# Kernel optimization log

Hardware: AMD Instinct MI355X
Metric: run time of the kernel (lower is better)

## Reference

```python
import jax, jax.numpy as jnp
import numpy as np

PATCH = 8
C1 = 1e-4
C2 = 1e-3
EPS = 1e-3
ALPHA = 0.4
WEIGHTS = (1.0, 0.01, 1.0)


def charbonnier(x):
    return (x * x + EPS * EPS) ** ALPHA


def resize_bilinear_ac(img, H2, W2):
    # bilinear resize with align_corners=True (matches F.interpolate)
    B, C, H, W = img.shape
    fy = jnp.arange(H2, dtype=img.dtype) * ((H - 1) / max(H2 - 1, 1))
    fx = jnp.arange(W2, dtype=img.dtype) * ((W - 1) / max(W2 - 1, 1))
    y0 = jnp.clip(jnp.floor(fy).astype(jnp.int32), 0, H - 2)
    x0 = jnp.clip(jnp.floor(fx).astype(jnp.int32), 0, W - 2)
    wy = (fy - y0)[None, None, :, None]
    wx = (fx - x0)[None, None, None, :]
    rows = img[:, :, y0, :] * (1 - wy) + img[:, :, y0 + 1, :] * wy  # [B,C,H2,W]
    out = rows[:, :, :, x0] * (1 - wx) + rows[:, :, :, x0 + 1] * wx  # [B,C,H2,W2]
    return out


def bilinear_warp(img, flow):
    # backward warp: sample img at (x + u, y + v), bilinear, border clamp
    B, C, H, W = img.shape
    gx = jnp.arange(W, dtype=img.dtype)[None, None, :] + flow[:, 0]  # [B,H,W]
    gy = jnp.arange(H, dtype=img.dtype)[None, :, None] + flow[:, 1]  # [B,H,W]
    x0f = jnp.floor(gx)
    y0f = jnp.floor(gy)
    wx = (gx - x0f)[:, None]  # [B,1,H,W]
    wy = (gy - y0f)[:, None]
    x0 = jnp.clip(x0f.astype(jnp.int32), 0, W - 1)
    x1 = jnp.clip(x0 + 1, 0, W - 1)
    y0 = jnp.clip(y0f.astype(jnp.int32), 0, H - 1)
    y1 = jnp.clip(y0 + 1, 0, H - 1)
    imgf = img.reshape(B, C, H * W)

    def gather(yi, xi):
        idx = (yi * W + xi).reshape(B, 1, H * W)
        g = jnp.take_along_axis(imgf, jnp.broadcast_to(idx, (B, C, H * W)), axis=2)
        return g.reshape(B, C, H, W)

    v00 = gather(y0, x0)
    v01 = gather(y0, x1)
    v10 = gather(y1, x0)
    v11 = gather(y1, x1)
    top = v00 * (1 - wx) + v01 * wx
    bot = v10 * (1 - wx) + v11 * wx
    return top * (1 - wy) + bot * wy


def torch_gradient(x, axis):
    # torch.gradient: central diff interior, one-sided at edges, spacing 1
    n = x.shape[axis]
    sl = lambda a, b: jax.lax.slice_in_dim(x, a, b, axis=axis)
    first = sl(1, 2) - sl(0, 1)
    interior = (sl(2, n) - sl(0, n - 2)) * 0.5
    last = sl(n - 1, n) - sl(n - 2, n - 1)
    return jnp.concatenate([first, interior, last], axis=axis)


def ssim_score(I1, I2):
    # faithful to SSIMLoss: stats pooled over ALL non-overlapping patches per
    # (batch, channel), i.e. over the region cropped to multiples of patch.
    B, C, H, W = I1.shape
    p = min(PATCH, H)
    PH, PW = H // p, W // p
    x = I1[:, :, :PH * p, :PW * p].reshape(B, C, -1)
    y = I2[:, :, :PH * p, :PW * p].reshape(B, C, -1)
    N = x.shape[-1]
    mu1 = x.mean(-1)
    mu2 = y.mean(-1)
    d1 = x - mu1[..., None]
    d2 = y - mu2[..., None]
    var1 = (d1 * d1).sum(-1) / (N - 1)  # torch .var() is unbiased
    var2 = (d2 * d2).sum(-1) / (N - 1)
    s12 = (d1 * d2).mean(-1)
    num = (2 * mu1 * mu2 + C1) * (2 * s12 + C2)
    den = (mu1 ** 2 + mu2 ** 2 + C1) * (var1 + var2 + C2)
    return num / den  # [B, C]


def setup_inputs() -> dict:
    key = jax.random.key(0)
    k1, k2 = jax.random.split(key)
    images = jax.random.uniform(k1, (16, 33, 256, 256), dtype=jnp.float32)
    flows = jax.random.normal(k2, (16, 20, 128, 128), dtype=jnp.float32)
    return {"images": images, "flows": flows}


def reference(images, flows):
    B, Cf, FH, FW = flows.shape
    n_flows = Cf // 2  # 10 frame pairs
    imgs = resize_bilinear_ac(images, FH, FW)  # [B,33,FH,FW]
    src = imgs[:, 3:].reshape(B * n_flows, 3, FH, FW)
    fl = flows.reshape(B * n_flows, 2, FH, FW)
    warped = bilinear_warp(src, fl).reshape(B, n_flows * 3, FH, FW)
    ref = imgs[:, : n_flows * 3]

    similarity_loss = ssim_score(ref, warped).mean()

    flow_x = flows[:, 0::2]
    flow_y = flows[:, 1::2]
    smooth = (charbonnier(torch_gradient(flow_x, 1))
              + charbonnier(torch_gradient(flow_x, 2))
              + charbonnier(torch_gradient(flow_y, 1))
              + charbonnier(torch_gradient(flow_y, 2))).mean()

    pixel_loss = charbonnier(ref - warped).mean()

    return WEIGHTS[0] * pixel_loss + WEIGHTS[1] * smooth + WEIGHTS[2] * similarity_loss
```

## Files before the change

### kernel.cpp

```cpp
#include <hip/hip_runtime.h>

#define IH 256
#define IW 256
#define FH 128
#define FW 128
#define NB 16
#define ICH 33
#define NF 10
#define NC 30
#define PL (FH * FW)
#define RES_OFF 4096
#define RES_CNT (NB * ICH * PL)
#define WS_NEED ((size_t)(RES_OFF + RES_CNT) * 4)

__device__ __forceinline__ float charb(float g) {
    float t = fmaf(g, g, 1e-6f);
    return __builtin_amdgcn_exp2f(0.4f * __builtin_amdgcn_logf(t));
}

__device__ __forceinline__ float resized_at(const float* __restrict__ plane, int Y, int X) {
    const float s = (float)(255.0 / 127.0);
    float fy = (float)Y * s;
    float fx = (float)X * s;
    int y0 = (int)fy; y0 = y0 > IH - 2 ? IH - 2 : y0;
    int x0 = (int)fx; x0 = x0 > IW - 2 ? IW - 2 : x0;
    float wy = fy - (float)y0;
    float wx = fx - (float)x0;
    const float* p0 = plane + y0 * IW + x0;
    float v00 = p0[0], v01 = p0[1];
    float v10 = p0[IW], v11 = p0[IW + 1];
    float r0 = v00 * (1.f - wy) + v10 * wy;
    float r1 = v01 * (1.f - wy) + v11 * wy;
    return r0 * (1.f - wx) + r1 * wx;
}

__global__ void __launch_bounds__(256) resize_kernel(const float* __restrict__ images,
                                                     float* __restrict__ resized)
{
    int idx = blockIdx.x * 256 + threadIdx.x;
    int bc = idx >> 14;
    int pix = idx & (PL - 1);
    int h = pix >> 7;
    int w = pix & (FW - 1);
    const float* plane = images + (size_t)bc * (IH * IW);
    resized[idx] = resized_at(plane, h, w);
}

#define SPLIT 4
#define PIX_PER_BLOCK (PL / SPLIT)
__global__ void __launch_bounds__(256) loss_main(const float* __restrict__ resized,
                                                 const float* __restrict__ flows,
                                                 float* __restrict__ acc_bc,
                                                 float* __restrict__ acc_g)
{
    int bc = blockIdx.x / SPLIT;
    int part = blockIdx.x % SPLIT;
    int b = bc / NC;
    int c = bc % NC;
    int f = c / 3;
    const float* ref_plane = resized + (size_t)(b * ICH + c) * PL;
    const float* src_plane = resized + (size_t)(b * ICH + 3 + c) * PL;
    const float* fx_plane  = flows + (size_t)(b * 2 * NF + 2 * f) * PL;
    const float* fy_plane  = fx_plane + PL;

    float s_ref = 0.f, s_w = 0.f, s_r2 = 0.f, s_w2 = 0.f, s_rw = 0.f, s_pix = 0.f;
    int base = part * PIX_PER_BLOCK;
    for (int i = threadIdx.x; i < PIX_PER_BLOCK; i += 256) {
        int pix = base + i;
        int h = pix >> 7;
        int w = pix & (FW - 1);
        float ref = ref_plane[pix];
        float fxv = fx_plane[pix];
        float fyv = fy_plane[pix];
        float gx = (float)w + fxv;
        float gy = (float)h + fyv;
        float x0f = floorf(gx), y0f = floorf(gy);
        float wx = gx - x0f, wy = gy - y0f;
        int x0 = (int)x0f; x0 = min(max(x0, 0), FW - 1);
        int y0 = (int)y0f; y0 = min(max(y0, 0), FH - 1);
        int x1 = min(x0 + 1, FW - 1);
        int y1 = min(y0 + 1, FH - 1);
        const float* r0p = src_plane + y0 * FW;
        const float* r1p = src_plane + y1 * FW;
        float v00 = r0p[x0], v01 = r0p[x1];
        float v10 = r1p[x0], v11 = r1p[x1];
        float top = v00 * (1.f - wx) + v01 * wx;
        float bot = v10 * (1.f - wx) + v11 * wx;
        float wv = top * (1.f - wy) + bot * wy;

        s_ref += ref; s_w += wv;
        s_r2 += ref * ref; s_w2 += wv * wv; s_rw += ref * wv;
        s_pix += charb(ref - wv);
    }
    for (int off = 32; off > 0; off >>= 1) {
        s_ref += __shfl_down(s_ref, off, 64);
        s_w   += __shfl_down(s_w, off, 64);
        s_r2  += __shfl_down(s_r2, off, 64);
        s_w2  += __shfl_down(s_w2, off, 64);
        s_rw  += __shfl_down(s_rw, off, 64);
        s_pix += __shfl_down(s_pix, off, 64);
    }
    __shared__ float sh[4][6];
    int wave = threadIdx.x >> 6;
    if ((threadIdx.x & 63) == 0) {
        sh[wave][0] = s_ref; sh[wave][1] = s_w; sh[wave][2] = s_r2;
        sh[wave][3] = s_w2;  sh[wave][4] = s_rw; sh[wave][5] = s_pix;
    }
    __syncthreads();
    if (threadIdx.x == 0) {
        float t0 = 0, t1 = 0, t2 = 0, t3 = 0, t4 = 0, t5 = 0;
        for (int v = 0; v < 4; v++) {
            t0 += sh[v][0]; t1 += sh[v][1]; t2 += sh[v][2];
            t3 += sh[v][3]; t4 += sh[v][4]; t5 += sh[v][5];
        }
        float* a = acc_bc + bc * 8;
        atomicAdd(a + 0, t0);
        atomicAdd(a + 1, t1);
        atomicAdd(a + 2, t2);
        atomicAdd(a + 3, t3);
        atomicAdd(a + 4, t4);
        atomicAdd(acc_g + 0, t5);
    }
}

__global__ void __launch_bounds__(256) smooth_kernel(const float* __restrict__ flows,
                                                     float* __restrict__ acc_g)
{
    const int total = NB * NF * PL;
    float s = 0.f;
    for (int i = blockIdx.x * blockDim.x + threadIdx.x; i < total;
         i += gridDim.x * blockDim.x) {
        int w = i & (FW - 1);
        int h = (i >> 7) & (FH - 1);
        int f = (i >> 14) % NF;
        int b = i / (NF * PL);
        int pix = h * FW + w;
        const float* xp = flows + (size_t)(b * 2 * NF + 2 * f) * PL;
        const float* yp = xp + PL;

        float g1x, g1y;
        if (f == 0)           { g1x = xp[2 * PL + pix] - xp[pix];
                                g1y = yp[2 * PL + pix] - yp[pix]; }
        else if (f == NF - 1) { g1x = xp[pix] - xp[pix - 2 * PL];
                                g1y = yp[pix] - yp[pix - 2 * PL]; }
        else                  { g1x = 0.5f * (xp[2 * PL + pix] - xp[pix - 2 * PL]);
                                g1y = 0.5f * (yp[2 * PL + pix] - yp[pix - 2 * PL]); }

        float g2x, g2y;
        if (h == 0)           { g2x = xp[pix + FW] - xp[pix];
                                g2y = yp[pix + FW] - yp[pix]; }
        else if (h == FH - 1) { g2x = xp[pix] - xp[pix - FW];
                                g2y = yp[pix] - yp[pix - FW]; }
        else                  { g2x = 0.5f * (xp[pix + FW] - xp[pix - FW]);
                                g2y = 0.5f * (yp[pix + FW] - yp[pix - FW]); }

        s += charb(g1x) + charb(g2x) + charb(g1y) + charb(g2y);
    }
    for (int off = 32; off > 0; off >>= 1) s += __shfl_down(s, off, 64);
    __shared__ float sh[4];
    int wave = threadIdx.x >> 6;
    if ((threadIdx.x & 63) == 0) sh[wave] = s;
    __syncthreads();
    if (threadIdx.x == 0)
        atomicAdd(acc_g + 2, sh[0] + sh[1] + sh[2] + sh[3]);
}

__global__ void __launch_bounds__(512) finalize(const float* __restrict__ acc_bc,
                                                const float* __restrict__ acc_g,
                                                float* __restrict__ out)
{
    __shared__ float sh[512];
    int tid = threadIdx.x;
    float ssim = 0.f;
    if (tid < NB * NC) {
        const float* a = acc_bc + tid * 8;
        const float N = (float)PL;
        float mu1 = a[0] / N, mu2 = a[1] / N;
        float var1 = (a[2] - a[0] * mu1) / (N - 1.f);
        float var2 = (a[3] - a[1] * mu2) / (N - 1.f);
        float s12 = a[4] / N - mu1 * mu2;
        float num = (2.f * mu1 * mu2 + 1e-4f) * (2.f * s12 + 1e-3f);
        float den = (mu1 * mu1 + mu2 * mu2 + 1e-4f) * (var1 + var2 + 1e-3f);
        ssim = num / den;
    }
    sh[tid] = ssim;
    __syncthreads();
    for (int off = 256; off > 0; off >>= 1) {
        if (tid < off) sh[tid] += sh[tid + off];
        __syncthreads();
    }
    if (tid == 0) {
        float pix    = acc_g[0] / (float)(NB * NC * PL);
        float smooth = acc_g[2] / (float)(NB * NF * PL);
        float sim    = sh[0] / (float)(NB * NC);
        out[0] = pix + 0.01f * smooth + sim;
    }
}

__global__ void __launch_bounds__(256) loss_main_fb(const float* __restrict__ images,
                                                    const float* __restrict__ flows,
                                                    float* __restrict__ acc_bc,
                                                    float* __restrict__ acc_g)
{
    int bc = blockIdx.x / 8;
    int part = blockIdx.x % 8;
    int b = bc / NC;
    int c = bc % NC;
    int f = c / 3;
    const float* ref_plane = images + (size_t)(b * ICH + c) * (IH * IW);
    const float* src_plane = images + (size_t)(b * ICH + 3 + c) * (IH * IW);
    const float* fx_plane  = flows + (size_t)(b * 2 * NF + 2 * f) * PL;
    const float* fy_plane  = fx_plane + PL;

    float s_ref = 0.f, s_w = 0.f, s_r2 = 0.f, s_w2 = 0.f, s_rw = 0.f, s_pix = 0.f;
    int base = part * (PL / 8);
    for (int i = threadIdx.x; i < PL / 8; i += 256) {
        int pix = base + i;
        int h = pix >> 7;
        int w = pix & (FW - 1);
        float ref = resized_at(ref_plane, h, w);
        float fxv = fx_plane[pix];
        float fyv = fy_plane[pix];
        float gx = (float)w + fxv;
        float gy = (float)h + fyv;
        float x0f = floorf(gx), y0f = floorf(gy);
        float wx = gx - x0f, wy = gy - y0f;
        int x0 = (int)x0f; x0 = min(max(x0, 0), FW - 1);
        int y0 = (int)y0f; y0 = min(max(y0, 0), FH - 1);
        int x1 = min(x0 + 1, FW - 1);
        int y1 = min(y0 + 1, FH - 1);
        float v00 = resized_at(src_plane, y0, x0);
        float v01 = resized_at(src_plane, y0, x1);
        float v10 = resized_at(src_plane, y1, x0);
        float v11 = resized_at(src_plane, y1, x1);
        float top = v00 * (1.f - wx) + v01 * wx;
        float bot = v10 * (1.f - wx) + v11 * wx;
        float wv = top * (1.f - wy) + bot * wy;
        s_ref += ref; s_w += wv;
        s_r2 += ref * ref; s_w2 += wv * wv; s_rw += ref * wv;
        s_pix += charb(ref - wv);
    }
    for (int off = 32; off > 0; off >>= 1) {
        s_ref += __shfl_down(s_ref, off, 64);
        s_w   += __shfl_down(s_w, off, 64);
        s_r2  += __shfl_down(s_r2, off, 64);
        s_w2  += __shfl_down(s_w2, off, 64);
        s_rw  += __shfl_down(s_rw, off, 64);
        s_pix += __shfl_down(s_pix, off, 64);
    }
    if ((threadIdx.x & 63) == 0) {
        float* a = acc_bc + bc * 8;
        atomicAdd(a + 0, s_ref);
        atomicAdd(a + 1, s_w);
        atomicAdd(a + 2, s_r2);
        atomicAdd(a + 3, s_w2);
        atomicAdd(a + 4, s_rw);
        atomicAdd(acc_g + 0, s_pix);
    }
}

extern "C" void kernel_launch(void* const* d_in, const int* in_sizes, int n_in,
                              void* d_out, int out_size, void* d_ws, size_t ws_size,
                              hipStream_t stream) {
    const float* images = (const float*)d_in[0];
    const float* flows  = (const float*)d_in[1];
    float* acc_bc  = (float*)d_ws;
    float* acc_g   = acc_bc + NB * NC * 8;
    float* resized = (float*)d_ws + RES_OFF;
    (void)hipMemsetAsync(d_ws, 0, (NB * NC * 8 + 4) * sizeof(float), stream);
    if (ws_size >= WS_NEED) {
        resize_kernel<<<RES_CNT / 256, 256, 0, stream>>>(images, resized);
        loss_main<<<NB * NC * SPLIT, 256, 0, stream>>>(resized, flows, acc_bc, acc_g);
    } else {
        loss_main_fb<<<NB * NC * 8, 256, 0, stream>>>(images, flows, acc_bc, acc_g);
    }
    smooth_kernel<<<1280, 256, 0, stream>>>(flows, acc_g);
    finalize<<<1, 512, 0, stream>>>(acc_bc, acc_g, (float*)d_out);
}
```

Before: 277.5 us.

## Merge loss and smoothness kernels, fold accumulator zeroing into resize

The resize kernel now stages the four needed source rows in shared memory with float4 loads and zeroes the accumulators itself, which removes the memset. The warp-loss and smoothness passes become one launch, with block ranges assigned to each role, and the loss path handles two pixels per thread using float2 loads. The goal is to cut launch count and per-launch overhead and to let the two independent workloads overlap on the GPU. A possible cost is that loss blocks and smoothness blocks compete for the same resources within one grid.

```diff
diff --git a/kernel.cpp b/kernel.cpp
--- a/kernel.cpp
+++ b/kernel.cpp
@@ -9,6 +9,7 @@
 #define NF 10
 #define NC 30
 #define PL (FH * FW)
+#define ACC_FLOATS 3848
 #define RES_OFF 4096
 #define RES_CNT (NB * ICH * PL)
 #define WS_NEED ((size_t)(RES_OFF + RES_CNT) * 4)
@@ -16,6 +17,203 @@
 __device__ __forceinline__ float charb(float g) {
     float t = fmaf(g, g, 1e-6f);
     return __builtin_amdgcn_exp2f(0.4f * __builtin_amdgcn_logf(t));
+}
+
+__global__ void __launch_bounds__(256) resize_kernel(const float* __restrict__ images,
+                                                     float* __restrict__ resized,
+                                                     float* __restrict__ acc)
+{
+    if (blockIdx.x == 0) {
+        for (int i = threadIdx.x; i < ACC_FLOATS; i += 256) acc[i] = 0.f;
+    }
+    __shared__ float rows[4][256];
+    const float s = (float)(255.0 / 127.0);
+    int plane = blockIdx.x >> 6;
+    int j = blockIdx.x & 63;
+    int h0 = 2 * j;
+    int y0a = (int)((float)h0 * s);       if (y0a > IH - 2) y0a = IH - 2;
+    int y0b = (int)((float)(h0 + 1) * s); if (y0b > IH - 2) y0b = IH - 2;
+    int rowidx[4] = { y0a, y0a + 1, y0b, y0b + 1 };
+    const float* pin = images + (size_t)plane * (IH * IW);
+    int r = threadIdx.x >> 6;
+    int l = threadIdx.x & 63;
+    const float4* srcv = (const float4*)(pin + rowidx[r] * IW);
+    ((float4*)rows[r])[l] = srcv[l];
+    __syncthreads();
+    int lr = threadIdx.x >> 7;
+    int w = threadIdx.x & 127;
+    int h = h0 + lr;
+    float fy = (float)h * s;
+    int y0 = lr ? y0b : y0a;
+    float wy = fy - (float)y0;
+    float fx = (float)w * s;
+    int x0 = (int)fx; if (x0 > IW - 2) x0 = IW - 2;
+    float wx = fx - (float)x0;
+    float v00 = rows[2 * lr][x0],     v01 = rows[2 * lr][x0 + 1];
+    float v10 = rows[2 * lr + 1][x0], v11 = rows[2 * lr + 1][x0 + 1];
+    float r0 = v00 * (1.f - wy) + v10 * wy;
+    float r1 = v01 * (1.f - wy) + v11 * wy;
+    resized[(size_t)plane * PL + h * FW + w] = r0 * (1.f - wx) + r1 * wx;
+}
+
+__device__ __forceinline__ float warp_sample(const float* __restrict__ src_plane,
+                                             float gx, float gy) {
+    float x0f = floorf(gx), y0f = floorf(gy);
+    float wx = gx - x0f, wy = gy - y0f;
+    int x0 = (int)x0f; x0 = min(max(x0, 0), FW - 1);
+    int y0 = (int)y0f; y0 = min(max(y0, 0), FH - 1);
+    int x1 = min(x0 + 1, FW - 1);
+    int y1 = min(y0 + 1, FH - 1);
+    const float* r0p = src_plane + y0 * FW;
+    const float* r1p = src_plane + y1 * FW;
+    float v00 = r0p[x0], v01 = r0p[x1];
+    float v10 = r1p[x0], v11 = r1p[x1];
+    float top = v00 * (1.f - wx) + v01 * wx;
+    float bot = v10 * (1.f - wx) + v11 * wx;
+    return top * (1.f - wy) + bot * wy;
+}
+
+#define SPLIT 4
+#define LOSS_BLOCKS (NB * NC * SPLIT)
+#define SMOOTH_BLOCKS 1280
+#define PIX_PER_BLOCK (PL / SPLIT)
+__global__ void __launch_bounds__(256) fat_kernel(const float* __restrict__ resized,
+                                                  const float* __restrict__ flows,
+                                                  float* __restrict__ acc_bc,
+                                                  float* __restrict__ acc_g)
+{
+    if (blockIdx.x < LOSS_BLOCKS) {
+        int bc = blockIdx.x / SPLIT;
+        int part = blockIdx.x % SPLIT;
+        int b = bc / NC;
+        int c = bc % NC;
+        int f = c / 3;
+        const float* ref_plane = resized + (size_t)(b * ICH + c) * PL;
+        const float* src_plane = resized + (size_t)(b * ICH + 3 + c) * PL;
+        const float* fx_plane  = flows + (size_t)(b * 2 * NF + 2 * f) * PL;
+        const float* fy_plane  = fx_plane + PL;
+
+        float s_ref = 0.f, s_w = 0.f, s_r2 = 0.f, s_w2 = 0.f, s_rw = 0.f, s_pix = 0.f;
+        int base2 = part * (PIX_PER_BLOCK / 2);
+        for (int i = threadIdx.x; i < PIX_PER_BLOCK / 2; i += 256) {
+            int pix2 = base2 + i;
+            int pix = pix2 * 2;
+            int h = pix >> 7;
+            int w = pix & (FW - 1);
+            float2 ref2 = ((const float2*)ref_plane)[pix2];
+            float2 fx2  = ((const float2*)fx_plane)[pix2];
+            float2 fy2  = ((const float2*)fy_plane)[pix2];
+
+            float wv0 = warp_sample(src_plane, (float)w + fx2.x,       (float)h + fy2.x);
+            float wv1 = warp_sample(src_plane, (float)(w + 1) + fx2.y, (float)h + fy2.y);
+
+            s_ref += ref2.x + ref2.y;
+            s_w   += wv0 + wv1;
+            s_r2  += ref2.x * ref2.x + ref2.y * ref2.y;
+            s_w2  += wv0 * wv0 + wv1 * wv1;
+            s_rw  += ref2.x * wv0 + ref2.y * wv1;
+            s_pix += charb(ref2.x - wv0) + charb(ref2.y - wv1);
+        }
+        for (int off = 32; off > 0; off >>= 1) {
+            s_ref += __shfl_down(s_ref, off, 64);
+            s_w   += __shfl_down(s_w, off, 64);
+            s_r2  += __shfl_down(s_r2, off, 64);
+            s_w2  += __shfl_down(s_w2, off, 64);
+            s_rw  += __shfl_down(s_rw, off, 64);
+            s_pix += __shfl_down(s_pix, off, 64);
+        }
+        __shared__ float sh[4][6];
+        int wave = threadIdx.x >> 6;
+        if ((threadIdx.x & 63) == 0) {
+            sh[wave][0] = s_ref; sh[wave][1] = s_w; sh[wave][2] = s_r2;
+            sh[wave][3] = s_w2;  sh[wave][4] = s_rw; sh[wave][5] = s_pix;
+        }
+        __syncthreads();
+        if (threadIdx.x == 0) {
+            float t0 = 0, t1 = 0, t2 = 0, t3 = 0, t4 = 0, t5 = 0;
+            for (int v = 0; v < 4; v++) {
+                t0 += sh[v][0]; t1 += sh[v][1]; t2 += sh[v][2];
+                t3 += sh[v][3]; t4 += sh[v][4]; t5 += sh[v][5];
+            }
+            float* a = acc_bc + bc * 8;
+            atomicAdd(a + 0, t0);
+            atomicAdd(a + 1, t1);
+            atomicAdd(a + 2, t2);
+            atomicAdd(a + 3, t3);
+            atomicAdd(a + 4, t4);
+            atomicAdd(acc_g + 0, t5);
+        }
+    } else {
+        const int total = NB * NF * PL;
+        float s = 0.f;
+        for (int i = (blockIdx.x - LOSS_BLOCKS) * 256 + threadIdx.x; i < total;
+             i += SMOOTH_BLOCKS * 256) {
+            int w = i & (FW - 1);
+            int h = (i >> 7) & (FH - 1);
+            int f = (i >> 14) % NF;
+            int b = i / (NF * PL);
+            int pix = h * FW + w;
+            const float* xp = flows + (size_t)(b * 2 * NF + 2 * f) * PL;
+            const float* yp = xp + PL;
+
+            float g1x, g1y;
+            if (f == 0)           { g1x = xp[2 * PL + pix] - xp[pix];
+                                    g1y = yp[2 * PL + pix] - yp[pix]; }
+            else if (f == NF - 1) { g1x = xp[pix] - xp[pix - 2 * PL];
+                                    g1y = yp[pix] - yp[pix - 2 * PL]; }
+            else                  { g1x = 0.5f * (xp[2 * PL + pix] - xp[pix - 2 * PL]);
+                                    g1y = 0.5f * (yp[2 * PL + pix] - yp[pix - 2 * PL]); }
+
+            float g2x, g2y;
+            if (h == 0)           { g2x = xp[pix + FW] - xp[pix];
+                                    g2y = yp[pix + FW] - yp[pix]; }
+            else if (h == FH - 1) { g2x = xp[pix] - xp[pix - FW];
+                                    g2y = yp[pix] - yp[pix - FW]; }
+            else                  { g2x = 0.5f * (xp[pix + FW] - xp[pix - FW]);
+                                    g2y = 0.5f * (yp[pix + FW] - yp[pix - FW]); }
+
+            s += charb(g1x) + charb(g2x) + charb(g1y) + charb(g2y);
+        }
+        for (int off = 32; off > 0; off >>= 1) s += __shfl_down(s, off, 64);
+        __shared__ float shs[4];
+        int wave = threadIdx.x >> 6;
+        if ((threadIdx.x & 63) == 0) shs[wave] = s;
+        __syncthreads();
+        if (threadIdx.x == 0)
+            atomicAdd(acc_g + 2, shs[0] + shs[1] + shs[2] + shs[3]);
+    }
+}
+
+__global__ void __launch_bounds__(512) finalize(const float* __restrict__ acc_bc,
+                                                const float* __restrict__ acc_g,
+                                                float* __restrict__ out)
+{
+    __shared__ float sh[512];
+    int tid = threadIdx.x;
+    float ssim = 0.f;
+    if (tid < NB * NC) {
+        const float* a = acc_bc + tid * 8;
+        const float N = (float)PL;
+        float mu1 = a[0] / N, mu2 = a[1] / N;
+        float var1 = (a[2] - a[0] * mu1) / (N - 1.f);
+        float var2 = (a[3] - a[1] * mu2) / (N - 1.f);
+        float s12 = a[4] / N - mu1 * mu2;
+        float num = (2.f * mu1 * mu2 + 1e-4f) * (2.f * s12 + 1e-3f);
+        float den = (mu1 * mu1 + mu2 * mu2 + 1e-4f) * (var1 + var2 + 1e-3f);
+        ssim = num / den;
+    }
+    sh[tid] = ssim;
+    __syncthreads();
+    for (int off = 256; off > 0; off >>= 1) {
+        if (tid < off) sh[tid] += sh[tid + off];
+        __syncthreads();
+    }
+    if (tid == 0) {
+        float pix    = acc_g[0] / (float)(NB * NC * PL);
+        float smooth = acc_g[2] / (float)(NB * NF * PL);
+        float sim    = sh[0] / (float)(NB * NC);
+        out[0] = pix + 0.01f * smooth + sim;
+    }
 }
 
 __device__ __forceinline__ float resized_at(const float* __restrict__ plane, int Y, int X) {
@@ -32,169 +230,6 @@
     float r0 = v00 * (1.f - wy) + v10 * wy;
     float r1 = v01 * (1.f - wy) + v11 * wy;
     return r0 * (1.f - wx) + r1 * wx;
-}
-
-__global__ void __launch_bounds__(256) resize_kernel(const float* __restrict__ images,
-                                                     float* __restrict__ resized)
-{
-    int idx = blockIdx.x * 256 + threadIdx.x;
-    int bc = idx >> 14;
-    int pix = idx & (PL - 1);
-    int h = pix >> 7;
-    int w = pix & (FW - 1);
-    const float* plane = images + (size_t)bc * (IH * IW);
-    resized[idx] = resized_at(plane, h, w);
-}
-
-#define SPLIT 4
-#define PIX_PER_BLOCK (PL / SPLIT)
-__global__ void __launch_bounds__(256) loss_main(const float* __restrict__ resized,
-                                                 const float* __restrict__ flows,
-                                                 float* __restrict__ acc_bc,
-                                                 float* __restrict__ acc_g)
-{
-    int bc = blockIdx.x / SPLIT;
-    int part = blockIdx.x % SPLIT;
-    int b = bc / NC;
-    int c = bc % NC;
-    int f = c / 3;
-    const float* ref_plane = resized + (size_t)(b * ICH + c) * PL;
-    const float* src_plane = resized + (size_t)(b * ICH + 3 + c) * PL;
-    const float* fx_plane  = flows + (size_t)(b * 2 * NF + 2 * f) * PL;
-    const float* fy_plane  = fx_plane + PL;
-
-    float s_ref = 0.f, s_w = 0.f, s_r2 = 0.f, s_w2 = 0.f, s_rw = 0.f, s_pix = 0.f;
-    int base = part * PIX_PER_BLOCK;
-    for (int i = threadIdx.x; i < PIX_PER_BLOCK; i += 256) {
-        int pix = base + i;
-        int h = pix >> 7;
-        int w = pix & (FW - 1);
-        float ref = ref_plane[pix];
-        float fxv = fx_plane[pix];
-        float fyv = fy_plane[pix];
-        float gx = (float)w + fxv;
-        float gy = (float)h + fyv;
-        float x0f = floorf(gx), y0f = floorf(gy);
-        float wx = gx - x0f, wy = gy - y0f;
-        int x0 = (int)x0f; x0 = min(max(x0, 0), FW - 1);
-        int y0 = (int)y0f; y0 = min(max(y0, 0), FH - 1);
-        int x1 = min(x0 + 1, FW - 1);
-        int y1 = min(y0 + 1, FH - 1);
-        const float* r0p = src_plane + y0 * FW;
-        const float* r1p = src_plane + y1 * FW;
-        float v00 = r0p[x0], v01 = r0p[x1];
-        float v10 = r1p[x0], v11 = r1p[x1];
-        float top = v00 * (1.f - wx) + v01 * wx;
-        float bot = v10 * (1.f - wx) + v11 * wx;
-        float wv = top * (1.f - wy) + bot * wy;
-
-        s_ref += ref; s_w += wv;
-        s_r2 += ref * ref; s_w2 += wv * wv; s_rw += ref * wv;
-        s_pix += charb(ref - wv);
-    }
-    for (int off = 32; off > 0; off >>= 1) {
-        s_ref += __shfl_down(s_ref, off, 64);
-        s_w   += __shfl_down(s_w, off, 64);
-        s_r2  += __shfl_down(s_r2, off, 64);
-        s_w2  += __shfl_down(s_w2, off, 64);
-        s_rw  += __shfl_down(s_rw, off, 64);
-        s_pix += __shfl_down(s_pix, off, 64);
-    }
-    __shared__ float sh[4][6];
-    int wave = threadIdx.x >> 6;
-    if ((threadIdx.x & 63) == 0) {
-        sh[wave][0] = s_ref; sh[wave][1] = s_w; sh[wave][2] = s_r2;
-        sh[wave][3] = s_w2;  sh[wave][4] = s_rw; sh[wave][5] = s_pix;
-    }
-    __syncthreads();
-    if (threadIdx.x == 0) {
-        float t0 = 0, t1 = 0, t2 = 0, t3 = 0, t4 = 0, t5 = 0;
-        for (int v = 0; v < 4; v++) {
-            t0 += sh[v][0]; t1 += sh[v][1]; t2 += sh[v][2];
-            t3 += sh[v][3]; t4 += sh[v][4]; t5 += sh[v][5];
-        }
-        float* a = acc_bc + bc * 8;
-        atomicAdd(a + 0, t0);
-        atomicAdd(a + 1, t1);
-        atomicAdd(a + 2, t2);
-        atomicAdd(a + 3, t3);
-        atomicAdd(a + 4, t4);
-        atomicAdd(acc_g + 0, t5);
-    }
-}
-
-__global__ void __launch_bounds__(256) smooth_kernel(const float* __restrict__ flows,
-                                                     float* __restrict__ acc_g)
-{
-    const int total = NB * NF * PL;
-    float s = 0.f;
-    for (int i = blockIdx.x * blockDim.x + threadIdx.x; i < total;
-         i += gridDim.x * blockDim.x) {
-        int w = i & (FW - 1);
-        int h = (i >> 7) & (FH - 1);
-        int f = (i >> 14) % NF;
-        int b = i / (NF * PL);
-        int pix = h * FW + w;
-        const float* xp = flows + (size_t)(b * 2 * NF + 2 * f) * PL;
-        const float* yp = xp + PL;
-
-        float g1x, g1y;
-        if (f == 0)           { g1x = xp[2 * PL + pix] - xp[pix];
-                                g1y = yp[2 * PL + pix] - yp[pix]; }
-        else if (f == NF - 1) { g1x = xp[pix] - xp[pix - 2 * PL];
-                                g1y = yp[pix] - yp[pix - 2 * PL]; }
-        else                  { g1x = 0.5f * (xp[2 * PL + pix] - xp[pix - 2 * PL]);
-                                g1y = 0.5f * (yp[2 * PL + pix] - yp[pix - 2 * PL]); }
-
-        float g2x, g2y;
-        if (h == 0)           { g2x = xp[pix + FW] - xp[pix];
-                                g2y = yp[pix + FW] - yp[pix]; }
-        else if (h == FH - 1) { g2x = xp[pix] - xp[pix - FW];
-                                g2y = yp[pix] - yp[pix - FW]; }
-        else                  { g2x = 0.5f * (xp[pix + FW] - xp[pix - FW]);
-                                g2y = 0.5f * (yp[pix + FW] - yp[pix - FW]); }
-
-        s += charb(g1x) + charb(g2x) + charb(g1y) + charb(g2y);
-    }
-    for (int off = 32; off > 0; off >>= 1) s += __shfl_down(s, off, 64);
-    __shared__ float sh[4];
-    int wave = threadIdx.x >> 6;
-    if ((threadIdx.x & 63) == 0) sh[wave] = s;
-    __syncthreads();
-    if (threadIdx.x == 0)
-        atomicAdd(acc_g + 2, sh[0] + sh[1] + sh[2] + sh[3]);
-}
-
-__global__ void __launch_bounds__(512) finalize(const float* __restrict__ acc_bc,
-                                                const float* __restrict__ acc_g,
-                                                float* __restrict__ out)
-{
-    __shared__ float sh[512];
-    int tid = threadIdx.x;
-    float ssim = 0.f;
-    if (tid < NB * NC) {
-        const float* a = acc_bc + tid * 8;
-        const float N = (float)PL;
-        float mu1 = a[0] / N, mu2 = a[1] / N;
-        float var1 = (a[2] - a[0] * mu1) / (N - 1.f);
-        float var2 = (a[3] - a[1] * mu2) / (N - 1.f);
-        float s12 = a[4] / N - mu1 * mu2;
-        float num = (2.f * mu1 * mu2 + 1e-4f) * (2.f * s12 + 1e-3f);
-        float den = (mu1 * mu1 + mu2 * mu2 + 1e-4f) * (var1 + var2 + 1e-3f);
-        ssim = num / den;
-    }
-    sh[tid] = ssim;
-    __syncthreads();
-    for (int off = 256; off > 0; off >>= 1) {
-        if (tid < off) sh[tid] += sh[tid + off];
-        __syncthreads();
-    }
-    if (tid == 0) {
-        float pix    = acc_g[0] / (float)(NB * NC * PL);
-        float smooth = acc_g[2] / (float)(NB * NF * PL);
-        float sim    = sh[0] / (float)(NB * NC);
-        out[0] = pix + 0.01f * smooth + sim;
-    }
 }
 
 __global__ void __launch_bounds__(256) loss_main_fb(const float* __restrict__ images,
@@ -259,6 +294,44 @@
     }
 }
 
+__global__ void __launch_bounds__(256) smooth_fb(const float* __restrict__ flows,
+                                                 float* __restrict__ acc_g)
+{
+    const int total = NB * NF * PL;
+    float s = 0.f;
+    for (int i = blockIdx.x * 256 + threadIdx.x; i < total; i += 1280 * 256) {
+        int w = i & (FW - 1);
+        int h = (i >> 7) & (FH - 1);
+        int f = (i >> 14) % NF;
+        int b = i / (NF * PL);
+        int pix = h * FW + w;
+        const float* xp = flows + (size_t)(b * 2 * NF + 2 * f) * PL;
+        const float* yp = xp + PL;
+        float g1x, g1y;
+        if (f == 0)           { g1x = xp[2 * PL + pix] - xp[pix];
+                                g1y = yp[2 * PL + pix] - yp[pix]; }
+        else if (f == NF - 1) { g1x = xp[pix] - xp[pix - 2 * PL];
+                                g1y = yp[pix] - yp[pix - 2 * PL]; }
+        else                  { g1x = 0.5f * (xp[2 * PL + pix] - xp[pix - 2 * PL]);
+                                g1y = 0.5f * (yp[2 * PL + pix] - yp[pix - 2 * PL]); }
+        float g2x, g2y;
+        if (h == 0)           { g2x = xp[pix + FW] - xp[pix];
+                                g2y = yp[pix + FW] - yp[pix]; }
+        else if (h == FH - 1) { g2x = xp[pix] - xp[pix - FW];
+                                g2y = yp[pix] - yp[pix - FW]; }
+        else                  { g2x = 0.5f * (xp[pix + FW] - xp[pix - FW]);
+                                g2y = 0.5f * (yp[pix + FW] - yp[pix - FW]); }
+        s += charb(g1x) + charb(g2x) + charb(g1y) + charb(g2y);
+    }
+    for (int off = 32; off > 0; off >>= 1) s += __shfl_down(s, off, 64);
+    __shared__ float sh[4];
+    int wave = threadIdx.x >> 6;
+    if ((threadIdx.x & 63) == 0) sh[wave] = s;
+    __syncthreads();
+    if (threadIdx.x == 0)
+        atomicAdd(acc_g + 2, sh[0] + sh[1] + sh[2] + sh[3]);
+}
+
 extern "C" void kernel_launch(void* const* d_in, const int* in_sizes, int n_in,
                               void* d_out, int out_size, void* d_ws, size_t ws_size,
                               hipStream_t stream) {
@@ -267,13 +340,14 @@
     float* acc_bc  = (float*)d_ws;
     float* acc_g   = acc_bc + NB * NC * 8;
     float* resized = (float*)d_ws + RES_OFF;
-    (void)hipMemsetAsync(d_ws, 0, (NB * NC * 8 + 4) * sizeof(float), stream);
     if (ws_size >= WS_NEED) {
-        resize_kernel<<<RES_CNT / 256, 256, 0, stream>>>(images, resized);
-        loss_main<<<NB * NC * SPLIT, 256, 0, stream>>>(resized, flows, acc_bc, acc_g);
+        resize_kernel<<<NB * ICH * (FH / 2), 256, 0, stream>>>(images, resized, acc_bc);
+        fat_kernel<<<LOSS_BLOCKS + SMOOTH_BLOCKS, 256, 0, stream>>>(resized, flows,
+                                                                    acc_bc, acc_g);
     } else {
+        (void)hipMemsetAsync(d_ws, 0, ACC_FLOATS * sizeof(float), stream);
         loss_main_fb<<<NB * NC * 8, 256, 0, stream>>>(images, flows, acc_bc, acc_g);
-    }
-    smooth_kernel<<<1280, 256, 0, stream>>>(flows, acc_g);
+        smooth_fb<<<1280, 256, 0, stream>>>(flows, acc_g);
+    }
     finalize<<<1, 512, 0, stream>>>(acc_bc, acc_g, (float*)d_out);
 }
```

Result: faster. 261.6 us (-5.8%).
